# Kernel optimization log

Measured on AMD Instinct MI355X. Metric: run time of the kernel, lower is better.

## Reference

```python
import jax, jax.numpy as jnp
import numpy as np
import math

N, CH, T, S = 32, 64, 2048, 77  # batch*heads, per-head channels, query len, encoder len

def setup_inputs() -> dict:
    key = jax.random.key(0)
    k1, k2 = jax.random.split(key)
    qkv = jax.random.normal(k1, (N, 3 * CH, T), dtype=jnp.float32)
    encoder_kv = jax.random.normal(k2, (N, 2 * CH, S), dtype=jnp.float32)
    attn_mask = jnp.zeros((1, T, S + T), dtype=jnp.float32)
    return {"qkv": qkv, "encoder_kv": encoder_kv, "attn_mask": attn_mask}

def reference(qkv, encoder_kv, attn_mask):
    ch = qkv.shape[1] // 3
    q, k, v = jnp.split(qkv, 3, axis=1)          # each [N, ch, T]
    ek, ev = jnp.split(encoder_kv, 2, axis=1)    # each [N, ch, S]
    k = jnp.concatenate([ek, k], axis=-1)        # [N, ch, S+T]
    v = jnp.concatenate([ev, v], axis=-1)
    scale = 1.0 / math.sqrt(math.sqrt(ch))
    weight = jnp.einsum('bct,bcs->bts', q * scale, k * scale)  # [N, T, S+T]
    weight = weight.astype(jnp.float32) + attn_mask
    weight = jax.nn.softmax(weight, axis=-1).astype(v.dtype)
    return jnp.einsum('bts,bcs->bct', weight, v)  # [N, ch, T]
```

## Files before the change

kernel.cpp:

```cpp
#include <hip/hip_runtime.h>


typedef __attribute__((ext_vector_type(8))) __bf16 bf16x8;
typedef __attribute__((ext_vector_type(8))) unsigned short u16x8;
typedef __attribute__((ext_vector_type(4))) float f32x4;
typedef float f32x4a __attribute__((ext_vector_type(4))) __attribute__((aligned(4)));
typedef __attribute__((ext_vector_type(4))) unsigned u32x4;
typedef __attribute__((ext_vector_type(2))) unsigned u32x2;

#define L2E  1.44269504089f
#define NEGM (-23.0830936f)

static __device__ __forceinline__ unsigned short f2bf(float f) {
    unsigned u = __builtin_bit_cast(unsigned, f);
    u += 0x7fffu + ((u >> 16) & 1u);
    return (unsigned short)(u >> 16);
}

static __device__ __forceinline__ unsigned pack_bf16(float a, float b) {
#if __has_builtin(__builtin_amdgcn_cvt_pk_bf16_f32)
    typedef __bf16 bf16x2_t __attribute__((ext_vector_type(2)));
    bf16x2_t r = __builtin_amdgcn_cvt_pk_bf16_f32(a, b);
    unsigned u; __builtin_memcpy(&u, &r, 4);
    return u;
#else
    unsigned ua = __builtin_bit_cast(unsigned, a);
    unsigned ub = __builtin_bit_cast(unsigned, b);
    ua += 0x7fffu + ((ua >> 16) & 1u);
    ub += 0x7fffu + ((ub >> 16) & 1u);
    return __builtin_amdgcn_perm(ub, ua, 0x07060302u);
#endif
}

__global__ __launch_bounds__(256) void prep_all(const float* __restrict__ qkv,
                                                const float* __restrict__ ekv,
                                                unsigned short* __restrict__ kws,
                                                unsigned short* __restrict__ vws,
                                                const float* __restrict__ mask) {
    int b = blockIdx.x;
    int tid = threadIdx.x;

    if (b >= 3136) {
        int bb = b - 3136;
        const u32x4* m4 = (const u32x4*)mask;
        unsigned acc = 0;
        for (int i = (bb << 8) + tid; i < 1088000; i += 131072) {
            u32x4 x = m4[i];
            acc |= x.x | x.y | x.z | x.w;
        }
        if (acc) atomicOr((unsigned*)(kws + (size_t)2175 * 64), 1u);
        return;
    }

    if (b >= 1088) {
        int bb = b - 1088;
        int n = bb >> 6, c = bb & 63;
        const float* v  = qkv + (size_t)n * 192 * 2048 + (size_t)(128 + c) * 2048;
        const float* ev = ekv + (size_t)n * 128 * 77 + (size_t)(64 + c) * 77;
        unsigned short* dst = vws + ((size_t)n * 64 + c) * 2176;
        for (int u = tid; u < 544; u += 256) {
            int s = u << 2;
            float f[4];
            if (u >= 20 && u <= 530) {
                f32x4a x = *(const f32x4a*)(v + s - 77);
                f[0] = x.x; f[1] = x.y; f[2] = x.z; f[3] = x.w;
            } else {
                #pragma unroll
                for (int k = 0; k < 4; ++k) {
                    int sk = s + k;
                    f[k] = (sk < 77) ? ev[sk] : ((sk < 2125) ? v[sk - 77] : 0.f);
                }
            }
            u32x2 pk; pk.x = pack_bf16(f[0], f[1]); pk.y = pack_bf16(f[2], f[3]);
            *(u32x2*)(dst + s) = pk;
        }
        return;
    }

    __shared__ float tile[64][65];
    int mode, n, t0;
    if (b < 1024) { mode = 1; n = b >> 5;          t0 = (b & 31) << 6; }
    else          { mode = 2; n = (b - 1024) >> 1; t0 = ((b - 1024) & 1) << 6; }

    const float* src;
    size_t srow;
    int tmax = 64;
    if (mode == 1) { src = qkv + (size_t)n * 192 * 2048 + (size_t)64 * 2048 + t0; srow = 2048; }
    else           { src = ekv + (size_t)n * 128 * 77 + t0; srow = 77;
                     tmax = 77 - t0; if (tmax > 64) tmax = 64; }

    #pragma unroll
    for (int i = 0; i < 4; ++i) {
        int idx = tid + (i << 8);
        int c  = idx >> 4;
        int t4 = (idx & 15) << 2;
        const float* p = src + (size_t)c * srow + t4;
        float v0, v1, v2, v3;
        if (mode == 1) {
            f32x4 v = *(const f32x4*)p;
            v0 = v.x; v1 = v.y; v2 = v.z; v3 = v.w;
        } else {
            v0 = (t4 + 0 < tmax) ? p[0] : 0.f;
            v1 = (t4 + 1 < tmax) ? p[1] : 0.f;
            v2 = (t4 + 2 < tmax) ? p[2] : 0.f;
            v3 = (t4 + 3 < tmax) ? p[3] : 0.f;
        }
        tile[t4 + 0][c] = v0;
        tile[t4 + 1][c] = v1;
        tile[t4 + 2][c] = v2;
        tile[t4 + 3][c] = v3;
    }
    __syncthreads();
    #pragma unroll
    for (int i = 0; i < 4; ++i) {
        int idx = tid + (i << 8);
        int row = idx >> 4;
        int c4  = (idx & 15) << 2;
        if (mode == 2 && row >= tmax) continue;
        u32x2 pk;
        pk.x = pack_bf16(tile[row][c4 + 0], tile[row][c4 + 1]);
        pk.y = pack_bf16(tile[row][c4 + 2], tile[row][c4 + 3]);
        unsigned short* dst;
        if (mode == 1) dst = kws + ((size_t)n * 2176 + 77 + t0 + row) * 64;
        else           dst = kws + ((size_t)n * 2176 + t0 + row) * 64;
        *(u32x2*)(dst + c4) = pk;
    }
}

__global__ __launch_bounds__(256, 2) void flash_attn(
        const float* __restrict__ qkv,
        const unsigned short* __restrict__ kws,
        const unsigned short* __restrict__ vws,
        const float* __restrict__ mask,
        float* __restrict__ out) {
    __shared__ alignas(16) unsigned short k_lds[2][64 * 72];
    __shared__ alignas(16) unsigned short v_lds[3][64 * 72];
    __shared__ alignas(16) unsigned short p_lds[4][32 * 72];

    const int n    = blockIdx.y;
    const int t0   = blockIdx.x << 7;
    const int tid  = threadIdx.x;
    const int wave = tid >> 6;
    const int lane = tid & 63;
    const int q    = lane >> 4;
    const int l16  = lane & 15;
    const int tc0  = t0 + (wave << 5) + l16;
    const int tc1  = tc0 + 16;

    const bool domask =
        __builtin_amdgcn_readfirstlane(*(const unsigned*)(kws + (size_t)2175 * 64)) != 0u;

    bf16x8 qf[2][2];
    #pragma unroll
    for (int h = 0; h < 2; ++h) {
        const float* qsrc = qkv + (size_t)n * 192 * 2048 + (h ? tc1 : tc0);
        u16x8 a0, a1;
        #pragma unroll
        for (int j = 0; j < 8; ++j) {
            a0[j] = f2bf(qsrc[(size_t)((q << 3) + j) * 2048] * 0.125f);
            a1[j] = f2bf(qsrc[(size_t)(32 + (q << 3) + j) * 2048] * 0.125f);
        }
        qf[h][0] = __builtin_bit_cast(bf16x8, a0);
        qf[h][1] = __builtin_bit_cast(bf16x8, a1);
    }

    bf16x8 ones;
    {
        u16x8 o;
        #pragma unroll
        for (int j = 0; j < 8; ++j) o[j] = 0x3F80;
        ones = __builtin_bit_cast(bf16x8, o);
    }

    const float* mrow0 = mask + (size_t)tc0 * 2125;
    const float* mrow1 = mask + (size_t)tc1 * 2125;
    unsigned short* const pw0 = p_lds[wave] + (size_t)l16 * 72;
    unsigned short* const pw1 = p_lds[wave] + (size_t)(16 + l16) * 72;

    const int srow0 = tid >> 3,        sch = (tid & 7) << 3;
    const int srow1 = srow0 + 32;

    const unsigned short* kp0 = kws + (size_t)n * 2176 * 64 + (size_t)srow0 * 64 + sch;
    const unsigned short* kp1 = kws + (size_t)n * 2176 * 64 + (size_t)srow1 * 64 + sch;
    const unsigned short* vp0 = vws + (size_t)n * 64 * 2176 + (size_t)srow0 * 2176 + sch;
    const unsigned short* vp1 = vws + (size_t)n * 64 * 2176 + (size_t)srow1 * 2176 + sch;

    f32x4 of[2][4] = {};
    f32x4 lacc0 = {}, lacc1 = {};
    f32x4 sacc[4][2];

    u32x4 kreg[2], vreg[2];

    auto issue_kv = [&]() {
        kreg[0] = *(const u32x4*)kp0;
        vreg[0] = *(const u32x4*)vp0;
        kreg[1] = *(const u32x4*)kp1;
        vreg[1] = *(const u32x4*)vp1;
        kp0 += 4096; kp1 += 4096; vp0 += 64; vp1 += 64;
    };
    auto stage = [&](unsigned short* kb, unsigned short* vb) {
        *(u32x4*)(kb + srow0 * 72 + sch) = kreg[0];
        *(u32x4*)(vb + srow0 * 72 + sch) = vreg[0];
        *(u32x4*)(kb + srow1 * 72 + sch) = kreg[1];
        *(u32x4*)(vb + srow1 * 72 + sch) = vreg[1];
    };
    auto qkm = [&](const unsigned short* kb) {
        #pragma unroll
        for (int sm = 0; sm < 4; ++sm) {
            const unsigned short* kp = kb + (size_t)((sm << 4) + l16) * 72 + (q << 3);
            bf16x8 ak0 = *(const bf16x8*)(kp);
            bf16x8 ak1 = *(const bf16x8*)(kp + 32);
            #pragma unroll
            for (int h = 0; h < 2; ++h) {
                f32x4 a = {};
                a = __builtin_amdgcn_mfma_f32_16x16x32_bf16(ak0, qf[h][0], a, 0, 0, 0);
                a = __builtin_amdgcn_mfma_f32_16x16x32_bf16(ak1, qf[h][1], a, 0, 0, 0);
                sacc[sm][h] = a;
            }
        }
    };
    auto smax = [&](int s0) {
        const bool tail = (s0 + 64 > 2125);
        #pragma unroll
        for (int sm = 0; sm < 4; ++sm) {
            int sbase = s0 + (sm << 4) + (q << 2);
            #pragma unroll
            for (int h = 0; h < 2; ++h) {
                f32x4 a = sacc[sm][h];
                if (domask) {
                    int sclamp = sbase > 2121 ? 2121 : sbase;
                    f32x4a m = *(const f32x4a*)((h ? mrow1 : mrow0) + sclamp);
                    a[0] += m.x; a[1] += m.y; a[2] += m.z; a[3] += m.w;
                }
                if (tail) {
                    #pragma unroll
                    for (int j = 0; j < 4; ++j)
                        if (sbase + j >= 2125) a[j] = -1e30f;
                }
                float p0 = __builtin_amdgcn_exp2f(__builtin_fmaf(a[0], L2E, NEGM));
                float p1 = __builtin_amdgcn_exp2f(__builtin_fmaf(a[1], L2E, NEGM));
                float p2 = __builtin_amdgcn_exp2f(__builtin_fmaf(a[2], L2E, NEGM));
                float p3 = __builtin_amdgcn_exp2f(__builtin_fmaf(a[3], L2E, NEGM));
                u32x2 pk; pk.x = pack_bf16(p0, p1); pk.y = pack_bf16(p2, p3);
                *(u32x2*)((h ? pw1 : pw0) + (sm << 4) + (q << 2)) = pk;
            }
        }
    };
    auto pv = [&](const unsigned short* vb) {
        bf16x8 bp00 = *(const bf16x8*)(pw0 + (q << 3));
        bf16x8 bp01 = *(const bf16x8*)(pw0 + (q << 3) + 32);
        bf16x8 bp10 = *(const bf16x8*)(pw1 + (q << 3));
        bf16x8 bp11 = *(const bf16x8*)(pw1 + (q << 3) + 32);
        lacc0 = __builtin_amdgcn_mfma_f32_16x16x32_bf16(ones, bp00, lacc0, 0, 0, 0);
        lacc0 = __builtin_amdgcn_mfma_f32_16x16x32_bf16(ones, bp01, lacc0, 0, 0, 0);
        lacc1 = __builtin_amdgcn_mfma_f32_16x16x32_bf16(ones, bp10, lacc1, 0, 0, 0);
        lacc1 = __builtin_amdgcn_mfma_f32_16x16x32_bf16(ones, bp11, lacc1, 0, 0, 0);
        #pragma unroll
        for (int cm = 0; cm < 4; ++cm) {
            const unsigned short* vp = vb + (size_t)((cm << 4) + l16) * 72 + (q << 3);
            bf16x8 av0 = *(const bf16x8*)(vp);
            bf16x8 av1 = *(const bf16x8*)(vp + 32);
            of[0][cm] = __builtin_amdgcn_mfma_f32_16x16x32_bf16(av0, bp00, of[0][cm], 0, 0, 0);
            of[0][cm] = __builtin_amdgcn_mfma_f32_16x16x32_bf16(av1, bp01, of[0][cm], 0, 0, 0);
            of[1][cm] = __builtin_amdgcn_mfma_f32_16x16x32_bf16(av0, bp10, of[1][cm], 0, 0, 0);
            of[1][cm] = __builtin_amdgcn_mfma_f32_16x16x32_bf16(av1, bp11, of[1][cm], 0, 0, 0);
        }
    };

    issue_kv();
    stage(k_lds[0], v_lds[0]);
    __syncthreads();
    issue_kv();
    qkm(k_lds[0]);
    smax(0);

    int vri = 0, vwi = 1;
    for (int ks = 0; ks < 33; ++ks) {
        const int s1 = (ks + 1) << 6;
        stage(k_lds[(ks + 1) & 1], v_lds[vwi]);
        __syncthreads();
        if (ks < 32) issue_kv();
        qkm(k_lds[(ks + 1) & 1]);
        pv(v_lds[vri]);
        smax(s1);
        vri = (vri == 2) ? 0 : vri + 1;
        vwi = (vwi == 2) ? 0 : vwi + 1;
    }
    pv(v_lds[vri]);

    float inv0 = 1.0f / lacc0[0], inv1 = 1.0f / lacc1[0];
    #pragma unroll
    for (int cm = 0; cm < 4; ++cm)
        #pragma unroll
        for (int j = 0; j < 4; ++j) {
            int c = (cm << 4) + (q << 2) + j;
            float* o = out + ((size_t)n * 64 + c) * 2048;
            o[tc0] = of[0][cm][j] * inv0;
            o[tc1] = of[1][cm][j] * inv1;
        }
}

extern "C" void kernel_launch(void* const* d_in, const int* in_sizes, int n_in,
                              void* d_out, int out_size, void* d_ws, size_t ws_size,
                              hipStream_t stream) {
    const float* qkv  = (const float*)d_in[0];
    const float* ekv  = (const float*)d_in[1];
    const float* mask = (const float*)d_in[2];
    float* out = (float*)d_out;

    unsigned short* kws = (unsigned short*)d_ws;
    unsigned short* vws = kws + (size_t)32 * 2176 * 64;

    hipMemsetAsync((char*)d_ws + (size_t)2175 * 64 * 2, 0, 4, stream);
    prep_all<<<3648, 256, 0, stream>>>(qkv, ekv, kws, vws, mask);
    dim3 grid(16, 32);
    flash_attn<<<grid, 256, 0, stream>>>(qkv, kws, vws, mask, out);
}
```

Before: 157.4 us.

## Split key dimension across wave pairs with cross-wave output reduction

```diff
diff --git a/kernel.cpp b/kernel.cpp
--- a/kernel.cpp
+++ b/kernel.cpp
@@ -134,34 +134,35 @@
         const float* __restrict__ mask,
         float* __restrict__ out) {
     __shared__ alignas(16) unsigned short k_lds[2][64 * 72];
-    __shared__ alignas(16) unsigned short v_lds[3][64 * 72];
-    __shared__ alignas(16) unsigned short p_lds[4][32 * 72];
+    __shared__ alignas(16) unsigned short v_lds[2][64 * 72];
+    __shared__ alignas(16) unsigned short p_lds[4][64 * 40];
 
     const int n    = blockIdx.y;
     const int t0   = blockIdx.x << 7;
     const int tid  = threadIdx.x;
     const int wave = tid >> 6;
+    const int sh   = wave >> 1;
+    const int th   = wave & 1;
     const int lane = tid & 63;
     const int q    = lane >> 4;
     const int l16  = lane & 15;
-    const int tc0  = t0 + (wave << 5) + l16;
-    const int tc1  = tc0 + 16;
+    const int tcb  = t0 + (th << 6);
 
     const bool domask =
         __builtin_amdgcn_readfirstlane(*(const unsigned*)(kws + (size_t)2175 * 64)) != 0u;
 
-    bf16x8 qf[2][2];
-    #pragma unroll
-    for (int h = 0; h < 2; ++h) {
-        const float* qsrc = qkv + (size_t)n * 192 * 2048 + (h ? tc1 : tc0);
+    bf16x8 qf[4][2];
+    #pragma unroll
+    for (int tg = 0; tg < 4; ++tg) {
+        const float* qsrc = qkv + (size_t)n * 192 * 2048 + tcb + (tg << 4) + l16;
         u16x8 a0, a1;
         #pragma unroll
         for (int j = 0; j < 8; ++j) {
             a0[j] = f2bf(qsrc[(size_t)((q << 3) + j) * 2048] * 0.125f);
             a1[j] = f2bf(qsrc[(size_t)(32 + (q << 3) + j) * 2048] * 0.125f);
         }
-        qf[h][0] = __builtin_bit_cast(bf16x8, a0);
-        qf[h][1] = __builtin_bit_cast(bf16x8, a1);
+        qf[tg][0] = __builtin_bit_cast(bf16x8, a0);
+        qf[tg][1] = __builtin_bit_cast(bf16x8, a1);
     }
 
     bf16x8 ones;
@@ -172,12 +173,7 @@
         ones = __builtin_bit_cast(bf16x8, o);
     }
 
-    const float* mrow0 = mask + (size_t)tc0 * 2125;
-    const float* mrow1 = mask + (size_t)tc1 * 2125;
-    unsigned short* const pw0 = p_lds[wave] + (size_t)l16 * 72;
-    unsigned short* const pw1 = p_lds[wave] + (size_t)(16 + l16) * 72;
-
-    const int srow0 = tid >> 3,        sch = (tid & 7) << 3;
+    const int srow0 = tid >> 3, sch = (tid & 7) << 3;
     const int srow1 = srow0 + 32;
 
     const unsigned short* kp0 = kws + (size_t)n * 2176 * 64 + (size_t)srow0 * 64 + sch;
@@ -185,9 +181,12 @@
     const unsigned short* vp0 = vws + (size_t)n * 64 * 2176 + (size_t)srow0 * 2176 + sch;
     const unsigned short* vp1 = vws + (size_t)n * 64 * 2176 + (size_t)srow1 * 2176 + sch;
 
-    f32x4 of[2][4] = {};
-    f32x4 lacc0 = {}, lacc1 = {};
-    f32x4 sacc[4][2];
+    unsigned short* const pwl = p_lds[wave] + l16 * 40;
+    const unsigned short* const prd = p_lds[wave] + l16 * 40 + (q << 3);
+
+    f32x4 of[4][4] = {};
+    f32x4 lacc[4]  = {};
+    f32x4 sacc[2][4];
 
     u32x4 kreg[2], vreg[2];
 
@@ -206,30 +205,33 @@
     };
     auto qkm = [&](const unsigned short* kb) {
         #pragma unroll
-        for (int sm = 0; sm < 4; ++sm) {
-            const unsigned short* kp = kb + (size_t)((sm << 4) + l16) * 72 + (q << 3);
+        for (int sb = 0; sb < 2; ++sb) {
+            const unsigned short* kp =
+                kb + (size_t)((sh << 5) + (sb << 4) + l16) * 72 + (q << 3);
             bf16x8 ak0 = *(const bf16x8*)(kp);
             bf16x8 ak1 = *(const bf16x8*)(kp + 32);
             #pragma unroll
-            for (int h = 0; h < 2; ++h) {
+            for (int tg = 0; tg < 4; ++tg) {
                 f32x4 a = {};
-                a = __builtin_amdgcn_mfma_f32_16x16x32_bf16(ak0, qf[h][0], a, 0, 0, 0);
-                a = __builtin_amdgcn_mfma_f32_16x16x32_bf16(ak1, qf[h][1], a, 0, 0, 0);
-                sacc[sm][h] = a;
+                a = __builtin_amdgcn_mfma_f32_16x16x32_bf16(ak0, qf[tg][0], a, 0, 0, 0);
+                a = __builtin_amdgcn_mfma_f32_16x16x32_bf16(ak1, qf[tg][1], a, 0, 0, 0);
+                sacc[sb][tg] = a;
             }
         }
     };
     auto smax = [&](int s0) {
         const bool tail = (s0 + 64 > 2125);
         #pragma unroll
-        for (int sm = 0; sm < 4; ++sm) {
-            int sbase = s0 + (sm << 4) + (q << 2);
-            #pragma unroll
-            for (int h = 0; h < 2; ++h) {
-                f32x4 a = sacc[sm][h];
+        for (int sb = 0; sb < 2; ++sb) {
+            #pragma unroll
+            for (int tg = 0; tg < 4; ++tg) {
+                const int sbase = s0 + (sh << 5) + (sb << 4) + (q << 2);
+                f32x4 a = sacc[sb][tg];
                 if (domask) {
                     int sclamp = sbase > 2121 ? 2121 : sbase;
-                    f32x4a m = *(const f32x4a*)((h ? mrow1 : mrow0) + sclamp);
+                    const float* mrow =
+                        mask + (size_t)(tcb + (tg << 4) + l16) * 2125;
+                    f32x4a m = *(const f32x4a*)(mrow + sclamp);
                     a[0] += m.x; a[1] += m.y; a[2] += m.z; a[3] += m.w;
                 }
                 if (tail) {
@@ -242,62 +244,102 @@
                 float p2 = __builtin_amdgcn_exp2f(__builtin_fmaf(a[2], L2E, NEGM));
                 float p3 = __builtin_amdgcn_exp2f(__builtin_fmaf(a[3], L2E, NEGM));
                 u32x2 pk; pk.x = pack_bf16(p0, p1); pk.y = pack_bf16(p2, p3);
-                *(u32x2*)((h ? pw1 : pw0) + (sm << 4) + (q << 2)) = pk;
+                *(u32x2*)(pwl + tg * 640 + (sb << 4) + (q << 2)) = pk;
             }
         }
     };
     auto pv = [&](const unsigned short* vb) {
-        bf16x8 bp00 = *(const bf16x8*)(pw0 + (q << 3));
-        bf16x8 bp01 = *(const bf16x8*)(pw0 + (q << 3) + 32);
-        bf16x8 bp10 = *(const bf16x8*)(pw1 + (q << 3));
-        bf16x8 bp11 = *(const bf16x8*)(pw1 + (q << 3) + 32);
-        lacc0 = __builtin_amdgcn_mfma_f32_16x16x32_bf16(ones, bp00, lacc0, 0, 0, 0);
-        lacc0 = __builtin_amdgcn_mfma_f32_16x16x32_bf16(ones, bp01, lacc0, 0, 0, 0);
-        lacc1 = __builtin_amdgcn_mfma_f32_16x16x32_bf16(ones, bp10, lacc1, 0, 0, 0);
-        lacc1 = __builtin_amdgcn_mfma_f32_16x16x32_bf16(ones, bp11, lacc1, 0, 0, 0);
-        #pragma unroll
-        for (int cm = 0; cm < 4; ++cm) {
-            const unsigned short* vp = vb + (size_t)((cm << 4) + l16) * 72 + (q << 3);
-            bf16x8 av0 = *(const bf16x8*)(vp);
-            bf16x8 av1 = *(const bf16x8*)(vp + 32);
-            of[0][cm] = __builtin_amdgcn_mfma_f32_16x16x32_bf16(av0, bp00, of[0][cm], 0, 0, 0);
-            of[0][cm] = __builtin_amdgcn_mfma_f32_16x16x32_bf16(av1, bp01, of[0][cm], 0, 0, 0);
-            of[1][cm] = __builtin_amdgcn_mfma_f32_16x16x32_bf16(av0, bp10, of[1][cm], 0, 0, 0);
-            of[1][cm] = __builtin_amdgcn_mfma_f32_16x16x32_bf16(av1, bp11, of[1][cm], 0, 0, 0);
+        bf16x8 bp[4];
+        #pragma unroll
+        for (int tg = 0; tg < 4; ++tg)
+            bp[tg] = *(const bf16x8*)(prd + tg * 640);
+        #pragma unroll
+        for (int tg = 0; tg < 4; ++tg)
+            lacc[tg] = __builtin_amdgcn_mfma_f32_16x16x32_bf16(ones, bp[tg], lacc[tg], 0, 0, 0);
+        #pragma unroll
+        for (int cb = 0; cb < 4; ++cb) {
+            const unsigned short* vp =
+                vb + (size_t)((cb << 4) + l16) * 72 + (sh << 5) + (q << 3);
+            bf16x8 av = *(const bf16x8*)(vp);
+            #pragma unroll
+            for (int tg = 0; tg < 4; ++tg)
+                of[cb][tg] = __builtin_amdgcn_mfma_f32_16x16x32_bf16(av, bp[tg], of[cb][tg], 0, 0, 0);
         }
     };
 
     issue_kv();
-    stage(k_lds[0], v_lds[0]);
+    for (int ks = 0; ks < 34; ++ks) {
+        if (ks > 0) pv(v_lds[(ks - 1) & 1]);
+        stage(k_lds[ks & 1], v_lds[ks & 1]);
+        __syncthreads();
+        if (ks < 33) issue_kv();
+        qkm(k_lds[ks & 1]);
+        smax(ks << 6);
+    }
+    pv(v_lds[1]);
+
     __syncthreads();
-    issue_kv();
-    qkm(k_lds[0]);
-    smax(0);
-
-    int vri = 0, vwi = 1;
-    for (int ks = 0; ks < 33; ++ks) {
-        const int s1 = (ks + 1) << 6;
-        stage(k_lds[(ks + 1) & 1], v_lds[vwi]);
+    float* exA = (float*)(&p_lds[0][0]);
+    float* exB = exA + 2048;
+    const int xb = (th << 10) + (lane << 2);
+    #pragma unroll
+    for (int r = 0; r < 2; ++r) {
+        if (sh) {
+            #pragma unroll
+            for (int tg = 0; tg < 4; ++tg)
+                *(f32x4*)(exA + xb + (tg << 8)) = (r == 0) ? of[0][tg] : of[1][tg];
+        } else {
+            #pragma unroll
+            for (int tg = 0; tg < 4; ++tg)
+                *(f32x4*)(exB + xb + (tg << 8)) = (r == 0) ? of[2][tg] : of[3][tg];
+        }
         __syncthreads();
-        if (ks < 32) issue_kv();
-        qkm(k_lds[(ks + 1) & 1]);
-        pv(v_lds[vri]);
-        smax(s1);
-        vri = (vri == 2) ? 0 : vri + 1;
-        vwi = (vwi == 2) ? 0 : vwi + 1;
-    }
-    pv(v_lds[vri]);
-
-    float inv0 = 1.0f / lacc0[0], inv1 = 1.0f / lacc1[0];
-    #pragma unroll
-    for (int cm = 0; cm < 4; ++cm)
+        if (!sh) {
+            #pragma unroll
+            for (int tg = 0; tg < 4; ++tg) {
+                f32x4 x = *(const f32x4*)(exA + xb + (tg << 8));
+                if (r == 0) of[0][tg] += x; else of[1][tg] += x;
+            }
+        } else {
+            #pragma unroll
+            for (int tg = 0; tg < 4; ++tg) {
+                f32x4 x = *(const f32x4*)(exB + xb + (tg << 8));
+                if (r == 0) of[2][tg] += x; else of[3][tg] += x;
+            }
+        }
+        __syncthreads();
+    }
+    if (sh) {
+        #pragma unroll
+        for (int tg = 0; tg < 4; ++tg) *(f32x4*)(exA + xb + (tg << 8)) = lacc[tg];
+    } else {
+        #pragma unroll
+        for (int tg = 0; tg < 4; ++tg) *(f32x4*)(exB + xb + (tg << 8)) = lacc[tg];
+    }
+    __syncthreads();
+    if (!sh) {
+        #pragma unroll
+        for (int tg = 0; tg < 4; ++tg) lacc[tg] += *(const f32x4*)(exA + xb + (tg << 8));
+    } else {
+        #pragma unroll
+        for (int tg = 0; tg < 4; ++tg) lacc[tg] += *(const f32x4*)(exB + xb + (tg << 8));
+    }
+
+    const int cbase = sh << 5;
+    #pragma unroll
+    for (int tg = 0; tg < 4; ++tg) {
+        const float inv = 1.0f / lacc[tg][0];
+        const int t = tcb + (tg << 4) + l16;
+        f32x4 oA = sh ? of[2][tg] : of[0][tg];
+        f32x4 oB = sh ? of[3][tg] : of[1][tg];
         #pragma unroll
         for (int j = 0; j < 4; ++j) {
-            int c = (cm << 4) + (q << 2) + j;
-            float* o = out + ((size_t)n * 64 + c) * 2048;
-            o[tc0] = of[0][cm][j] * inv0;
-            o[tc1] = of[1][cm][j] * inv1;
-        }
+            int cA = cbase + (q << 2) + j;
+            int cB = cA + 16;
+            out[((size_t)n * 64 + cA) * 2048 + t] = oA[j] * inv;
+            out[((size_t)n * 64 + cB) * 2048 + t] = oB[j] * inv;
+        }
+    }
 }
 
 extern "C" void kernel_launch(void* const* d_in, const int* in_sizes, int n_in,
```

New measurement: 386.3 us. 145% more time.

## Stream K/V tiles into LDS with async global_load_lds and XOR-swizzled layout

Applied to the files above, without the earlier changes.

```diff
diff --git a/kernel.cpp b/kernel.cpp
--- a/kernel.cpp
+++ b/kernel.cpp
@@ -32,6 +32,13 @@
 #endif
 }
 
+static __device__ __forceinline__ void gload16(const unsigned short* g,
+                                               unsigned short* l) {
+    __builtin_amdgcn_global_load_lds(
+        (const __attribute__((address_space(1))) unsigned*)g,
+        (__attribute__((address_space(3))) unsigned*)l, 16, 0, 0);
+}
+
 __global__ __launch_bounds__(256) void prep_all(const float* __restrict__ qkv,
                                                 const float* __restrict__ ekv,
                                                 unsigned short* __restrict__ kws,
@@ -58,6 +65,7 @@
         const float* v  = qkv + (size_t)n * 192 * 2048 + (size_t)(128 + c) * 2048;
         const float* ev = ekv + (size_t)n * 128 * 77 + (size_t)(64 + c) * 77;
         unsigned short* dst = vws + ((size_t)n * 64 + c) * 2176;
+        const int cx = c & 7;
         for (int u = tid; u < 544; u += 256) {
             int s = u << 2;
             float f[4];
@@ -72,7 +80,8 @@
                 }
             }
             u32x2 pk; pk.x = pack_bf16(f[0], f[1]); pk.y = pack_bf16(f[2], f[3]);
-            *(u32x2*)(dst + s) = pk;
+            int s2 = (s & ~63) | ((((s >> 3) & 7) ^ cx) << 3) | (s & 4);
+            *(u32x2*)(dst + s2) = pk;
         }
         return;
     }
@@ -120,10 +129,10 @@
         u32x2 pk;
         pk.x = pack_bf16(tile[row][c4 + 0], tile[row][c4 + 1]);
         pk.y = pack_bf16(tile[row][c4 + 2], tile[row][c4 + 3]);
-        unsigned short* dst;
-        if (mode == 1) dst = kws + ((size_t)n * 2176 + 77 + t0 + row) * 64;
-        else           dst = kws + ((size_t)n * 2176 + t0 + row) * 64;
-        *(u32x2*)(dst + c4) = pk;
+        int row_s = (mode == 1) ? (77 + t0 + row) : (t0 + row);
+        unsigned short* dst = kws + ((size_t)n * 2176 + row_s) * 64;
+        int c4s = ((((c4 >> 3) ^ (row_s & 7)) << 3) | (c4 & 4));
+        *(u32x2*)(dst + c4s) = pk;
     }
 }
 
@@ -133,8 +142,8 @@
         const unsigned short* __restrict__ vws,
         const float* __restrict__ mask,
         float* __restrict__ out) {
-    __shared__ alignas(16) unsigned short k_lds[2][64 * 72];
-    __shared__ alignas(16) unsigned short v_lds[3][64 * 72];
+    __shared__ alignas(16) unsigned short k_lds[2][64 * 64];
+    __shared__ alignas(16) unsigned short v_lds[3][64 * 64];
     __shared__ alignas(16) unsigned short p_lds[4][32 * 72];
 
     const int n    = blockIdx.y;
@@ -177,39 +186,35 @@
     unsigned short* const pw0 = p_lds[wave] + (size_t)l16 * 72;
     unsigned short* const pw1 = p_lds[wave] + (size_t)(16 + l16) * 72;
 
-    const int srow0 = tid >> 3,        sch = (tid & 7) << 3;
-    const int srow1 = srow0 + 32;
-
-    const unsigned short* kp0 = kws + (size_t)n * 2176 * 64 + (size_t)srow0 * 64 + sch;
-    const unsigned short* kp1 = kws + (size_t)n * 2176 * 64 + (size_t)srow1 * 64 + sch;
-    const unsigned short* vp0 = vws + (size_t)n * 64 * 2176 + (size_t)srow0 * 2176 + sch;
-    const unsigned short* vp1 = vws + (size_t)n * 64 * 2176 + (size_t)srow1 * 2176 + sch;
+    const unsigned short* kc0 = kws + (size_t)n * 2176 * 64 + ((size_t)tid << 3);
+    const unsigned short* kc1 = kc0 + 2048;
+    const unsigned short* vc0 = vws + (size_t)n * 64 * 2176
+                               + (size_t)(tid >> 3) * 2176 + ((tid & 7) << 3);
+    const unsigned short* vc1 = vc0 + (size_t)32 * 2176;
+    unsigned short* const kd0 = (unsigned short*)k_lds[0] + ((size_t)tid << 3);
+    unsigned short* const vd0 = (unsigned short*)v_lds[0] + ((size_t)tid << 3);
 
     f32x4 of[2][4] = {};
     f32x4 lacc0 = {}, lacc1 = {};
     f32x4 sacc[4][2];
 
-    u32x4 kreg[2], vreg[2];
-
-    auto issue_kv = [&]() {
-        kreg[0] = *(const u32x4*)kp0;
-        vreg[0] = *(const u32x4*)vp0;
-        kreg[1] = *(const u32x4*)kp1;
-        vreg[1] = *(const u32x4*)vp1;
-        kp0 += 4096; kp1 += 4096; vp0 += 64; vp1 += 64;
-    };
-    auto stage = [&](unsigned short* kb, unsigned short* vb) {
-        *(u32x4*)(kb + srow0 * 72 + sch) = kreg[0];
-        *(u32x4*)(vb + srow0 * 72 + sch) = vreg[0];
-        *(u32x4*)(kb + srow1 * 72 + sch) = kreg[1];
-        *(u32x4*)(vb + srow1 * 72 + sch) = vreg[1];
+    auto stage_async = [&](int bk, int bv) {
+        unsigned short* kd = kd0 + bk * (64 * 64);
+        unsigned short* vd = vd0 + bv * (64 * 64);
+        gload16(kc0, kd);
+        gload16(kc1, kd + 2048);
+        gload16(vc0, vd);
+        gload16(vc1, vd + 2048);
+        kc0 += 4096; kc1 += 4096; vc0 += 64; vc1 += 64;
     };
     auto qkm = [&](const unsigned short* kb) {
+        const int ch0 = (q ^ (l16 & 7)) << 3;
+        __builtin_amdgcn_s_setprio(1);
         #pragma unroll
         for (int sm = 0; sm < 4; ++sm) {
-            const unsigned short* kp = kb + (size_t)((sm << 4) + l16) * 72 + (q << 3);
-            bf16x8 ak0 = *(const bf16x8*)(kp);
-            bf16x8 ak1 = *(const bf16x8*)(kp + 32);
+            const unsigned short* kp = kb + (size_t)((sm << 4) + l16) * 64;
+            bf16x8 ak0 = *(const bf16x8*)(kp + ch0);
+            bf16x8 ak1 = *(const bf16x8*)(kp + (ch0 ^ 32));
             #pragma unroll
             for (int h = 0; h < 2; ++h) {
                 f32x4 a = {};
@@ -218,6 +223,7 @@
                 sacc[sm][h] = a;
             }
         }
+        __builtin_amdgcn_s_setprio(0);
     };
     auto smax = [&](int s0) {
         const bool tail = (s0 + 64 > 2125);
@@ -247,46 +253,43 @@
         }
     };
     auto pv = [&](const unsigned short* vb) {
+        const int ch0 = (q ^ (l16 & 7)) << 3;
         bf16x8 bp00 = *(const bf16x8*)(pw0 + (q << 3));
         bf16x8 bp01 = *(const bf16x8*)(pw0 + (q << 3) + 32);
         bf16x8 bp10 = *(const bf16x8*)(pw1 + (q << 3));
         bf16x8 bp11 = *(const bf16x8*)(pw1 + (q << 3) + 32);
+        __builtin_amdgcn_s_setprio(1);
         lacc0 = __builtin_amdgcn_mfma_f32_16x16x32_bf16(ones, bp00, lacc0, 0, 0, 0);
         lacc0 = __builtin_amdgcn_mfma_f32_16x16x32_bf16(ones, bp01, lacc0, 0, 0, 0);
         lacc1 = __builtin_amdgcn_mfma_f32_16x16x32_bf16(ones, bp10, lacc1, 0, 0, 0);
         lacc1 = __builtin_amdgcn_mfma_f32_16x16x32_bf16(ones, bp11, lacc1, 0, 0, 0);
         #pragma unroll
         for (int cm = 0; cm < 4; ++cm) {
-            const unsigned short* vp = vb + (size_t)((cm << 4) + l16) * 72 + (q << 3);
-            bf16x8 av0 = *(const bf16x8*)(vp);
-            bf16x8 av1 = *(const bf16x8*)(vp + 32);
+            const unsigned short* vp = vb + (size_t)((cm << 4) + l16) * 64;
+            bf16x8 av0 = *(const bf16x8*)(vp + ch0);
+            bf16x8 av1 = *(const bf16x8*)(vp + (ch0 ^ 32));
             of[0][cm] = __builtin_amdgcn_mfma_f32_16x16x32_bf16(av0, bp00, of[0][cm], 0, 0, 0);
             of[0][cm] = __builtin_amdgcn_mfma_f32_16x16x32_bf16(av1, bp01, of[0][cm], 0, 0, 0);
             of[1][cm] = __builtin_amdgcn_mfma_f32_16x16x32_bf16(av0, bp10, of[1][cm], 0, 0, 0);
             of[1][cm] = __builtin_amdgcn_mfma_f32_16x16x32_bf16(av1, bp11, of[1][cm], 0, 0, 0);
         }
+        __builtin_amdgcn_s_setprio(0);
     };
 
-    issue_kv();
-    stage(k_lds[0], v_lds[0]);
+    stage_async(0, 0);
     __syncthreads();
-    issue_kv();
+    stage_async(1, 1);
     qkm(k_lds[0]);
     smax(0);
 
-    int vri = 0, vwi = 1;
-    for (int ks = 0; ks < 33; ++ks) {
-        const int s1 = (ks + 1) << 6;
-        stage(k_lds[(ks + 1) & 1], v_lds[vwi]);
+    for (int ks = 1; ks < 34; ++ks) {
         __syncthreads();
-        if (ks < 32) issue_kv();
-        qkm(k_lds[(ks + 1) & 1]);
-        pv(v_lds[vri]);
-        smax(s1);
-        vri = (vri == 2) ? 0 : vri + 1;
-        vwi = (vwi == 2) ? 0 : vwi + 1;
-    }
-    pv(v_lds[vri]);
+        if (ks < 33) stage_async((ks + 1) & 1, (ks + 1) % 3);
+        qkm(k_lds[ks & 1]);
+        pv(v_lds[(ks - 1) % 3]);
+        smax(ks << 6);
+    }
+    pv(v_lds[0]);
 
     float inv0 = 1.0f / lacc0[0], inv1 = 1.0f / lacc1[0];
     #pragma unroll
```

Result: no change. 158.6 us (+0.8%).
